# Performance work log

Hardware: AMD Instinct MI355X
Metric: run time of the kernel (lower is better)

The kernel has to match this reference:

```python
import jax, jax.numpy as jnp
import numpy as np
from jax import lax

NL, H, E, N, R, K, C, V, P = 8, 768, 1536, 16, 4, 4, 3, 256, 2048
EPS = 1e-5

def layernorm(x, w, b):
    m = jnp.mean(x, -1, keepdims=True)
    v = jnp.var(x, -1, keepdims=True)
    return (x - m) * lax.rsqrt(v + EPS) * w + b

def causal_dwconv(x, w, b):
    # x: [B,L,E], w: [E,K], b: [E]; causal depthwise conv (pad K-1 left, truncate)
    Bn, L, _ = x.shape
    xp = jnp.pad(x, ((0, 0), (K - 1, 0), (0, 0)))
    y = b
    acc = jnp.zeros_like(x)
    for j in range(K):
        acc = acc + xp[:, j:j + L, :] * w[:, j]
    return acc + b

def selective_scan(u, dt, Bm, Cm, A, Dv):
    # u,dt: [B,L,E]; Bm,Cm: [B,L,N]; A: [E,N]; Dv: [E]
    Bn = u.shape[0]
    def step(h, inp):
        u_t, dt_t, b_t, c_t = inp  # [B,E],[B,E],[B,N],[B,N]
        dA = jnp.exp(dt_t[:, :, None] * A)                      # [B,E,N]
        h = h * dA + (dt_t * u_t)[:, :, None] * b_t[:, None, :]
        y = jnp.einsum('ben,bn->be', h, c_t)
        return h, y
    h0 = jnp.zeros((Bn, E, N), dtype=u.dtype)
    xs = (u.transpose(1, 0, 2), dt.transpose(1, 0, 2),
          Bm.transpose(1, 0, 2), Cm.transpose(1, 0, 2))
    _, ys = lax.scan(step, h0, xs)
    return ys.transpose(1, 0, 2) + u * Dv

def mamba_block(hs, p):
    res = hs
    x = layernorm(hs, p['ln_w'], p['ln_b'])
    proj = x @ p['in_w'] + p['in_b']                            # [B,L,2E]
    xm, gate = proj[..., :E], proj[..., E:]
    xm = causal_dwconv(xm, p['conv_w'], p['conv_b'])
    u = jax.nn.silu(xm)                                         # swish activation in mixer
    dbc = u @ p['xproj_w']                                      # [B,L,R+2N]
    dt = jax.nn.softplus(dbc[..., :R] @ p['dt_w'] + p['dt_b'])  # [B,L,E]
    Bm, Cm = dbc[..., R:R + N], dbc[..., R + N:]
    A = -jnp.exp(p['A_log'])                                    # [E,N]
    y = selective_scan(u, dt, Bm, Cm, A, p['D'])
    y = jax.nn.sigmoid(gate) * y
    hs = y @ p['out_w'] + p['out_b'] + res
    # fractal layer: mean of recursive swish-linear branches, residual
    acc = jnp.zeros_like(hs)
    for i in range(C):
        yb = hs
        for _ in range(3):
            yb = jax.nn.silu(yb @ p['frac_w'][i] + p['frac_b'][i])
        acc = acc + yb
    return hs + 0.5 * acc / C

def setup_inputs() -> dict:
    key = jax.random.key(0)
    ks = jax.random.split(key, 20)
    s = lambda i, shp, sc=0.02: jax.random.normal(ks[i], shp, jnp.float32) * sc
    inp = {
        'input_ids': jax.random.randint(ks[0], (2, 2048), 0, V),
        'tok_emb': s(1, (V, H)),
        'pos_emb': s(2, (P, H)),
        'ln_w': jnp.ones((NL, H)), 'ln_b': jnp.zeros((NL, H)),
        'in_w': s(3, (NL, H, 2 * E)), 'in_b': jnp.zeros((NL, 2 * E)),
        'conv_w': s(4, (NL, E, K), 0.3), 'conv_b': jnp.zeros((NL, E)),
        'xproj_w': s(5, (NL, E, R + 2 * N)),
        'dt_w': s(6, (NL, R, E), 0.1),
        'dt_b': jnp.full((NL, E), -4.0),
        'A_log': jnp.tile(jnp.log(jnp.arange(1, N + 1, dtype=jnp.float32)), (NL, E, 1)),
        'D': jnp.ones((NL, E)),
        'out_w': s(7, (NL, E, H)), 'out_b': jnp.zeros((NL, H)),
        'frac_w': s(8, (NL, C, H, H)), 'frac_b': jnp.zeros((NL, C, H)),
        'fln_w': jnp.ones((H,)), 'fln_b': jnp.zeros((H,)),
    }
    return inp

def reference(input_ids, tok_emb, pos_emb, ln_w, ln_b, in_w, in_b, conv_w, conv_b,
              xproj_w, dt_w, dt_b, A_log, D, out_w, out_b, frac_w, frac_b, fln_w, fln_b):
    Bn, L = input_ids.shape
    hs = tok_emb[input_ids] + pos_emb[jnp.arange(L)][None]
    for l in range(NL):
        p = {'ln_w': ln_w[l], 'ln_b': ln_b[l], 'in_w': in_w[l], 'in_b': in_b[l],
             'conv_w': conv_w[l], 'conv_b': conv_b[l], 'xproj_w': xproj_w[l],
             'dt_w': dt_w[l], 'dt_b': dt_b[l], 'A_log': A_log[l], 'D': D[l],
             'out_w': out_w[l], 'out_b': out_b[l], 'frac_w': frac_w[l], 'frac_b': frac_b[l]}
        hs = mamba_block(hs, p)
    return layernorm(hs, fln_w, fln_b)
```

## Files before the change

kernel.cpp:

```cpp
#include <hip/hip_runtime.h>
#include <hip/hip_bf16.h>
#include <stdint.h>

#define NLAYER 8
#define HDIM   768
#define EDIM   1536
#define NST    16
#define LSEQ   2048
#define BATCH  2
#define BLTOK  (BATCH*LSEQ)
#define NCH    (BATCH*EDIM)
#define NCHK   64

typedef unsigned short u16;
typedef short  short8  __attribute__((ext_vector_type(8)));
typedef float  f32x4   __attribute__((ext_vector_type(4)));
typedef unsigned short u16x4 __attribute__((ext_vector_type(4)));

__device__ __forceinline__ float sigm(float x){ return 1.0f/(1.0f+__expf(-x)); }

__device__ __forceinline__ u16 bf16_rne(float x){
  unsigned u = __float_as_uint(x);
  return (u16)((u + 0x7fffu + ((u>>16)&1u)) >> 16);
}
__device__ __forceinline__ float bf16_f(u16 h){
  return __uint_as_float(((unsigned)h)<<16);
}

__device__ __forceinline__ void gload16(const void* g, void* l){
  __builtin_amdgcn_global_load_lds(
    reinterpret_cast<const __attribute__((address_space(1))) unsigned*>(
        reinterpret_cast<uintptr_t>(g)),
    reinterpret_cast<__attribute__((address_space(3))) unsigned*>(
        reinterpret_cast<uintptr_t>(l)),
    16, 0, 0);
}

__global__ __launch_bounds__(256) void wprep_k(
    const float* __restrict__ W, u16* __restrict__ H, u16* __restrict__ L,
    int Nsrc, int Ndst, int K)
{
  __shared__ float T[32][33];
  int z = blockIdx.z;
  W += (size_t)z*K*Nsrc; H += (size_t)z*Ndst*K; L += (size_t)z*Ndst*K;
  int n0 = blockIdx.x*32, k0 = blockIdx.y*32;
  int tx = threadIdx.x&31, ty = threadIdx.x>>5;
  #pragma unroll
  for (int r=0;r<4;r++){
    int kk = ty+8*r, col = n0+tx;
    T[kk][tx] = (col<Nsrc) ? W[(size_t)(k0+kk)*Nsrc+col] : 0.f;
  }
  __syncthreads();
  #pragma unroll
  for (int r=0;r<4;r++){
    int nn = ty+8*r, n = n0+nn, k = k0+tx;
    if (n<Ndst){
      float f = T[tx][nn];
      u16 h = bf16_rne(f);
      H[(size_t)n*K+k] = h;
      L[(size_t)n*K+k] = bf16_rne(f - bf16_f(h));
    }
  }
}

template<int EPI, int SPLIT, int SPLITK>
__global__ __launch_bounds__(256) void gemm_u(
    const u16* __restrict__ AH, const u16* __restrict__ AL, int lda,
    const u16* __restrict__ WH, const u16* __restrict__ WL, int ldw,
    const float* __restrict__ bias, void* __restrict__ Cout,
    int N, int Kloop, size_t zA, size_t zW, size_t zB, size_t zC)
{
  constexpr int NPL = (SPLIT==3)?4:2;
  __shared__ __align__(16) u16 smem[NPL*4096];
  u16* AsH = smem;
  u16* BsH = smem + 4096;
  u16* AsL = smem + 2*4096;
  u16* BsL = smem + 3*4096;

  const int z = blockIdx.z;
  const u16* ah = AH + (size_t)z*zA;
  const u16* bh = WH + (size_t)z*zW;
  const u16* al = nullptr;
  const u16* bl = nullptr;
  if constexpr (SPLIT==3){ al = AL + (size_t)z*zA; bl = WL + (size_t)z*zW; }

  const int tid  = threadIdx.x;
  const int m0 = blockIdx.y<<7, n0 = blockIdx.x<<7;
  const int wave = tid>>6, lane = tid&63;
  const int r = lane&15, q = lane>>4;
  const int wm = (wave&1)<<6, wn = (wave>>1)<<6;
  const int srow = tid>>2;
  const int scol = (tid&3)*8;
  const int sdst = tid*8;

  f32x4 acc[4][4];
  #pragma unroll
  for (int i=0;i<4;i++)
    #pragma unroll
    for (int j=0;j<4;j++)
      #pragma unroll
      for (int t=0;t<4;t++) acc[i][j][t]=0.f;

  for (int k0 = 0; k0 < Kloop; k0 += 32){
    #pragma unroll
    for (int i=0;i<2;i++){
      const size_t gao = (size_t)(m0 + i*64 + srow)*lda + k0 + scol;
      const size_t gbo = (size_t)(n0 + i*64 + srow)*ldw + k0 + scol;
      const int lo = i*2048 + sdst;
      gload16(ah+gao, AsH+lo);
      gload16(bh+gbo, BsH+lo);
      if constexpr (SPLIT==3){
        gload16(al+gao, AsL+lo);
        gload16(bl+gbo, BsL+lo);
      }
    }
    __syncthreads();

    short8 aHf[4], bHf[4];
    #pragma unroll
    for (int i=0;i<4;i++) aHf[i] = *(const short8*)&AsH[(wm + 16*i + r)*32 + q*8];
    #pragma unroll
    for (int j=0;j<4;j++) bHf[j] = *(const short8*)&BsH[(wn + 16*j + r)*32 + q*8];
    if constexpr (SPLIT==3){
      short8 aLf[4], bLf[4];
      #pragma unroll
      for (int i=0;i<4;i++) aLf[i] = *(const short8*)&AsL[(wm + 16*i + r)*32 + q*8];
      #pragma unroll
      for (int j=0;j<4;j++) bLf[j] = *(const short8*)&BsL[(wn + 16*j + r)*32 + q*8];
      #pragma unroll
      for (int i=0;i<4;i++)
        #pragma unroll
        for (int j=0;j<4;j++){
          acc[i][j] = __builtin_amdgcn_mfma_f32_16x16x32_bf16(aHf[i], bHf[j], acc[i][j], 0,0,0);
          acc[i][j] = __builtin_amdgcn_mfma_f32_16x16x32_bf16(aHf[i], bLf[j], acc[i][j], 0,0,0);
          acc[i][j] = __builtin_amdgcn_mfma_f32_16x16x32_bf16(aLf[i], bHf[j], acc[i][j], 0,0,0);
        }
    } else {
      #pragma unroll
      for (int i=0;i<4;i++)
        #pragma unroll
        for (int j=0;j<4;j++)
          acc[i][j] = __builtin_amdgcn_mfma_f32_16x16x32_bf16(aHf[i], bHf[j], acc[i][j], 0,0,0);
    }
    __syncthreads();
  }

  float* Cf = (float*)Cout + (size_t)z*zC;
  u16*   Cu = (u16*)Cout   + (size_t)z*zC;
  const float* bz = bias ? (bias + (size_t)z*zB) : bias;
  #pragma unroll
  for (int j=0;j<4;j++){
    int n_out = n0 + wn + 16*j + r;
    float bv = (bz && (!SPLITK || z==0)) ? bz[n_out] : 0.f;
    #pragma unroll
    for (int i=0;i<4;i++){
      #pragma unroll
      for (int reg=0;reg<4;reg++){
        int m_out = m0 + wm + 16*i + 4*q + reg;
        float v = acc[i][j][reg] + bv;
        if (EPI & 1) v *= sigm(v);
        size_t o = (size_t)m_out*N + n_out;
        if      (EPI & 16) atomicAdd(&Cf[o], v);
        else if (EPI & 8)  Cu[o] = bf16_rne(v);
        else if (EPI & 2)  Cf[o] += v;
        else               Cf[o] = v;
      }
    }
  }
}

__global__ __launch_bounds__(64) void xgemm_k(
    const float* __restrict__ A, const u16* __restrict__ XH,
    const u16* __restrict__ XL, float* __restrict__ DBC)
{
  int m0 = blockIdx.x*16;
  int lane = threadIdx.x;
  int r = lane&15, q = lane>>4;
  f32x4 acc[3];
  #pragma unroll
  for (int j=0;j<3;j++)
    #pragma unroll
    for (int t=0;t<4;t++) acc[j][t]=0.f;

  for (int k0 = 0; k0 < EDIM; k0 += 32){
    const float* ap = A + (size_t)(m0+r)*EDIM + k0 + q*8;
    float f[8];
    *(float4*)&f[0] = *(const float4*)(ap+0);
    *(float4*)&f[4] = *(const float4*)(ap+4);
    short8 ah, al;
    #pragma unroll
    for (int t=0;t<8;t++){
      u16 h = bf16_rne(f[t]);
      ah[t] = (short)h;
      al[t] = (short)bf16_rne(f[t]-bf16_f(h));
    }
    #pragma unroll
    for (int j=0;j<3;j++){
      size_t o = (size_t)(16*j+r)*EDIM + k0 + q*8;
      short8 bh = *(const short8*)&XH[o];
      short8 bl = *(const short8*)&XL[o];
      acc[j] = __builtin_amdgcn_mfma_f32_16x16x32_bf16(ah, bh, acc[j], 0,0,0);
      acc[j] = __builtin_amdgcn_mfma_f32_16x16x32_bf16(ah, bl, acc[j], 0,0,0);
      acc[j] = __builtin_amdgcn_mfma_f32_16x16x32_bf16(al, bh, acc[j], 0,0,0);
    }
  }
  #pragma unroll
  for (int j=0;j<3;j++){
    int n = 16*j + r;
    if (n < 36){
      #pragma unroll
      for (int reg=0;reg<4;reg++){
        int m = m0 + 4*q + reg;
        DBC[(size_t)m*36 + n] = acc[j][reg];
      }
    }
  }
}

__global__ __launch_bounds__(256) void embed_k(
    const int* __restrict__ ids, const float* __restrict__ tok,
    const float* __restrict__ pos, float* __restrict__ HS)
{
  int idx = blockIdx.x*256 + threadIdx.x;
  int h = idx % HDIM; int t = idx / HDIM;
  int lpos = t % LSEQ;
  int id = ids[t];
  HS[idx] = tok[id*HDIM + h] + pos[lpos*HDIM + h];
}

template<int PACK>
__global__ __launch_bounds__(256) void ln_k(
    const float* __restrict__ X, const float* __restrict__ w,
    const float* __restrict__ b, void* __restrict__ O1, void* __restrict__ O2)
{
  int t = blockIdx.x;
  const float* x = X + (size_t)t*HDIM;
  float s=0.f, s2=0.f;
  for (int i=threadIdx.x; i<HDIM; i+=256){ float v=x[i]; s+=v; s2+=v*v; }
  #pragma unroll
  for (int off=32; off; off>>=1){ s += __shfl_down(s,off,64); s2 += __shfl_down(s2,off,64); }
  __shared__ float rs[4], rs2[4], mv[2];
  int lane = threadIdx.x & 63, wv = threadIdx.x >> 6;
  if (!lane){ rs[wv]=s; rs2[wv]=s2; }
  __syncthreads();
  if (!threadIdx.x){
    float a = rs[0]+rs[1]+rs[2]+rs[3];
    float c = rs2[0]+rs2[1]+rs2[2]+rs2[3];
    float m = a/HDIM;
    mv[0]=m; mv[1]=rsqrtf(c/HDIM - m*m + 1e-5f);
  }
  __syncthreads();
  float m = mv[0], r = mv[1];
  for (int i=threadIdx.x; i<HDIM; i+=256){
    float v = (x[i]-m)*r*w[i] + b[i];
    if (PACK){
      u16 h = bf16_rne(v);
      ((u16*)O1)[(size_t)t*HDIM+i] = h;
      ((u16*)O2)[(size_t)t*HDIM+i] = bf16_rne(v - bf16_f(h));
    } else {
      ((float*)O1)[(size_t)t*HDIM+i] = v;
    }
  }
}

__global__ __launch_bounds__(256) void cvt_k(
    const float* __restrict__ X, u16* __restrict__ O)
{
  int i = blockIdx.x*256 + threadIdx.x;
  float4 v = ((const float4*)X)[i];
  u16x4 o;
  o[0]=bf16_rne(v.x); o[1]=bf16_rne(v.y); o[2]=bf16_rne(v.z); o[3]=bf16_rne(v.w);
  ((u16x4*)O)[i] = o;
}

__global__ __launch_bounds__(256) void conv_silu_k(
    const float* __restrict__ PROJ, const float* __restrict__ cw,
    const float* __restrict__ cb, float* __restrict__ U)
{
  int idx = blockIdx.x*256 + threadIdx.x;
  int e = idx % EDIM; int t = idx / EDIM;
  int l = t % LSEQ; int tb = t - l;
  float acc = cb[e];
  #pragma unroll
  for (int j=0;j<4;j++){
    int tt = l + j - 3;
    if (tt >= 0) acc += PROJ[(size_t)(tb+tt)*(2*EDIM) + e] * cw[e*4+j];
  }
  U[idx] = acc * sigm(acc);
}

__global__ __launch_bounds__(256) void scanA_k(
    const float* __restrict__ U, const float* __restrict__ DBC,
    const float* __restrict__ Alog, const float* __restrict__ dtw,
    const float* __restrict__ dtb, float* __restrict__ PSP,
    float* __restrict__ PSS)
{
  const int CH = LSEQ/NCHK;
  int el = threadIdx.x & 63, jj = threadIdx.x >> 6;
  int ch = blockIdx.x*64 + el;
  int j  = blockIdx.y*4 + jj;
  int e = ch % EDIM, b = ch / EDIM;

  float a[16], P[16], S[16];
  #pragma unroll
  for (int n=0;n<16;n++){ a[n] = -__expf(Alog[e*NST+n]); P[n]=1.f; S[n]=0.f; }
  float w0=dtw[e], w1=dtw[EDIM+e], w2=dtw[2*EDIM+e], w3=dtw[3*EDIM+e];
  float db=dtb[e];
  size_t base=(size_t)b*LSEQ;

  for (int t=j*CH; t<j*CH+CH; t++){
    size_t tok = base+t;
    float4 d4 = *(const float4*)&DBC[tok*36];
    float4 B0 = *(const float4*)&DBC[tok*36+4];
    float4 B1 = *(const float4*)&DBC[tok*36+8];
    float4 B2 = *(const float4*)&DBC[tok*36+12];
    float4 B3 = *(const float4*)&DBC[tok*36+16];
    float dt = d4.x*w0 + d4.y*w1 + d4.z*w2 + d4.w*w3 + db;
    dt = (dt>20.f)?dt:log1pf(__expf(dt));
    float du = dt * U[tok*EDIM+e];
    float Bv[16];
    *(float4*)&Bv[0]=B0; *(float4*)&Bv[4]=B1; *(float4*)&Bv[8]=B2; *(float4*)&Bv[12]=B3;
    #pragma unroll
    for (int n=0;n<16;n++){
      float dA = __expf(dt*a[n]);
      P[n]*=dA; S[n]=S[n]*dA + du*Bv[n];
    }
  }
  #pragma unroll
  for (int n=0;n<16;n++){
    PSP[(size_t)(j*16+n)*NCH + ch] = P[n];
    PSS[(size_t)(j*16+n)*NCH + ch] = S[n];
  }
}

__global__ __launch_bounds__(256) void scanB_k(
    const float* __restrict__ PSP, float* __restrict__ PSS)
{
  int idx = blockIdx.x*256 + threadIdx.x;
  int n = idx / NCH, ch = idx % NCH;
  float hin = 0.f;
  #pragma unroll 4
  for (int jj=0;jj<NCHK;jj++){
    size_t o = (size_t)(jj*16+n)*NCH + ch;
    float p = PSP[o], s = PSS[o];
    PSS[o] = hin;
    hin = p*hin + s;
  }
}

__global__ __launch_bounds__(256) void scanC_k(
    const float* __restrict__ U, const float* __restrict__ DBC,
    const float* __restrict__ Alog, const float* __restrict__ dtw,
    const float* __restrict__ dtb, const float* __restrict__ HIN,
    const float* __restrict__ Dp, const float* __restrict__ PROJ,
    u16* __restrict__ YH, u16* __restrict__ YL)
{
  const int CH = LSEQ/NCHK;
  int el = threadIdx.x & 63, jj = threadIdx.x >> 6;
  int ch = blockIdx.x*64 + el;
  int j  = blockIdx.y*4 + jj;
  int e = ch % EDIM, b = ch / EDIM;

  float a[16], h[16];
  #pragma unroll
  for (int n=0;n<16;n++){
    a[n] = -__expf(Alog[e*NST+n]);
    h[n] = HIN[(size_t)(j*16+n)*NCH + ch];
  }
  float w0=dtw[e], w1=dtw[EDIM+e], w2=dtw[2*EDIM+e], w3=dtw[3*EDIM+e];
  float db=dtb[e], dcf=Dp[e];
  size_t base=(size_t)b*LSEQ;

  for (int t=j*CH; t<j*CH+CH; t++){
    size_t tok = base+t;
    float4 d4 = *(const float4*)&DBC[tok*36];
    float4 B0 = *(const float4*)&DBC[tok*36+4];
    float4 B1 = *(const float4*)&DBC[tok*36+8];
    float4 B2 = *(const float4*)&DBC[tok*36+12];
    float4 B3 = *(const float4*)&DBC[tok*36+16];
    float4 C0 = *(const float4*)&DBC[tok*36+20];
    float4 C1 = *(const float4*)&DBC[tok*36+24];
    float4 C2 = *(const float4*)&DBC[tok*36+28];
    float4 C3 = *(const float4*)&DBC[tok*36+32];
    float dt = d4.x*w0 + d4.y*w1 + d4.z*w2 + d4.w*w3 + db;
    dt = (dt>20.f)?dt:log1pf(__expf(dt));
    float u = U[tok*EDIM+e];
    float du = dt * u;
    float Bv[16], Cv[16];
    *(float4*)&Bv[0]=B0; *(float4*)&Bv[4]=B1; *(float4*)&Bv[8]=B2; *(float4*)&Bv[12]=B3;
    *(float4*)&Cv[0]=C0; *(float4*)&Cv[4]=C1; *(float4*)&Cv[8]=C2; *(float4*)&Cv[12]=C3;
    float y = 0.f;
    #pragma unroll
    for (int n=0;n<16;n++){
      float dA = __expf(dt*a[n]);
      h[n] = h[n]*dA + du*Bv[n];
      y += h[n]*Cv[n];
    }
    float g = PROJ[tok*(2*EDIM) + EDIM + e];
    float yv = (y + u*dcf)*sigm(g);
    u16 hh = bf16_rne(yv);
    YH[tok*EDIM + e] = hh;
    YL[tok*EDIM + e] = bf16_rne(yv - bf16_f(hh));
  }
}

__global__ __launch_bounds__(256) void addscale3_k(
    float* __restrict__ HS, const float* __restrict__ FB)
{
  const size_t S = (size_t)BLTOK*HDIM;
  size_t i = blockIdx.x*256 + threadIdx.x;
  HS[i] += (FB[i] + FB[i+S] + FB[i+2*S]) * (0.5f/3.0f);
}

extern "C" void kernel_launch(void* const* d_in, const int* in_sizes, int n_in,
                              void* d_out, int out_size, void* d_ws, size_t ws_size,
                              hipStream_t stream)
{
  const int*   ids      = (const int*)d_in[0];
  const float* tok_emb  = (const float*)d_in[1];
  const float* pos_emb  = (const float*)d_in[2];
  const float* ln_w     = (const float*)d_in[3];
  const float* ln_b     = (const float*)d_in[4];
  const float* in_w     = (const float*)d_in[5];
  const float* in_b     = (const float*)d_in[6];
  const float* conv_w   = (const float*)d_in[7];
  const float* conv_b   = (const float*)d_in[8];
  const float* xproj_w  = (const float*)d_in[9];
  const float* dt_w     = (const float*)d_in[10];
  const float* dt_b     = (const float*)d_in[11];
  const float* A_log    = (const float*)d_in[12];
  const float* Dp       = (const float*)d_in[13];
  const float* out_w    = (const float*)d_in[14];
  const float* out_b    = (const float*)d_in[15];
  const float* frac_w   = (const float*)d_in[16];
  const float* frac_b   = (const float*)d_in[17];
  const float* fln_w    = (const float*)d_in[18];
  const float* fln_b    = (const float*)d_in[19];

  const size_t F_HS   = (size_t)BLTOK*HDIM;
  const size_t F_PROJ = (size_t)BLTOK*2*EDIM;
  const size_t F_R1   = (size_t)BLTOK*EDIM;
  float* HS   = (float*)d_ws;
  float* PROJ = HS   + F_HS;
  float* R1   = PROJ + F_PROJ;
  float* DBC  = R1   + F_R1;
  u16* W16  = (u16*)(DBC + (size_t)BLTOK*36);
  u16* inH  = W16;
  u16* inL  = inH  + (size_t)2359296;
  u16* outH = inL  + (size_t)2359296;
  u16* outL = outH + (size_t)1179648;
  u16* frH  = outL + (size_t)1179648;
  u16* frL  = frH  + (size_t)1769472;
  u16* xH   = frL  + (size_t)1769472;
  u16* xL   = xH   + (size_t)73728;
  float* PSP = (float*)(xL + (size_t)73728);
  float* PSS = PSP + (size_t)NCHK*16*NCH;
  u16* YH  = (u16*)(PSS + (size_t)NCHK*16*NCH);
  u16* YL  = YH + (size_t)BLTOK*EDIM;
  u16*   XH  = (u16*)R1;
  u16*   XL  = XH + F_HS;
  float* U   = R1;
  u16*   HSB = (u16*)PSP;
  float* FB  = PROJ;
  u16*   S1  = (u16*)(PROJ + 3*F_HS);
  u16*   S2  = S1 + 3*F_HS;

  embed_k<<<(BLTOK*HDIM)/256, 256, 0, stream>>>(ids, tok_emb, pos_emb, HS);

  const size_t zWf = (size_t)HDIM*HDIM;
  for (int l = 0; l < NLAYER; l++){
    wprep_k<<<dim3(3072/32, 768/32), 256, 0, stream>>>(
        in_w + (size_t)l*HDIM*2*EDIM, inH, inL, 2*EDIM, 2*EDIM, HDIM);
    wprep_k<<<dim3(768/32, 1536/32), 256, 0, stream>>>(
        out_w + (size_t)l*EDIM*HDIM, outH, outL, HDIM, HDIM, EDIM);
    wprep_k<<<dim3(768/32, 768/32, 3), 256, 0, stream>>>(
        frac_w + (size_t)l*3*HDIM*HDIM, frH, frL, HDIM, HDIM, HDIM);
    wprep_k<<<dim3(2, 1536/32), 256, 0, stream>>>(
        xproj_w + (size_t)l*EDIM*36, xH, xL, 36, 48, EDIM);

    ln_k<1><<<BLTOK, 256, 0, stream>>>(HS, ln_w + l*HDIM, ln_b + l*HDIM, XH, XL);

    gemm_u<0,3,0><<<dim3(24, 32), 256, 0, stream>>>(
        XH, XL, HDIM, inH, inL, HDIM, in_b + l*2*EDIM, PROJ,
        2*EDIM, HDIM, 0,0,0,0);

    conv_silu_k<<<(BLTOK*EDIM)/256, 256, 0, stream>>>(
        PROJ, conv_w + l*EDIM*4, conv_b + l*EDIM, U);

    xgemm_k<<<BLTOK/16, 64, 0, stream>>>(U, xH, xL, DBC);

    scanA_k<<<dim3(NCH/64, NCHK/4), 256, 0, stream>>>(
        U, DBC, A_log + (size_t)l*EDIM*NST, dt_w + (size_t)l*4*EDIM,
        dt_b + (size_t)l*EDIM, PSP, PSS);
    scanB_k<<<(NCH*16)/256, 256, 0, stream>>>(PSP, PSS);
    scanC_k<<<dim3(NCH/64, NCHK/4), 256, 0, stream>>>(
        U, DBC, A_log + (size_t)l*EDIM*NST, dt_w + (size_t)l*4*EDIM,
        dt_b + (size_t)l*EDIM, PSS, Dp + (size_t)l*EDIM, PROJ, YH, YL);

    gemm_u<16,3,1><<<dim3(6, 32, 2), 256, 0, stream>>>(
        YH, YL, EDIM, outH, outL, EDIM, out_b + l*HDIM, HS,
        HDIM, EDIM/2, EDIM/2, EDIM/2, 0, 0);

    cvt_k<<<(BLTOK*HDIM)/1024, 256, 0, stream>>>(HS, HSB);

    gemm_u<9,1,0><<<dim3(6, 32, 3), 256, 0, stream>>>(
        HSB, nullptr, HDIM, frH, frL, HDIM, frac_b + (size_t)l*3*HDIM, S1,
        HDIM, HDIM, 0, zWf, HDIM, F_HS);
    gemm_u<9,1,0><<<dim3(6, 32, 3), 256, 0, stream>>>(
        S1, nullptr, HDIM, frH, frL, HDIM, frac_b + (size_t)l*3*HDIM, S2,
        HDIM, HDIM, F_HS, zWf, HDIM, F_HS);
    gemm_u<1,1,0><<<dim3(6, 32, 3), 256, 0, stream>>>(
        S2, nullptr, HDIM, frH, frL, HDIM, frac_b + (size_t)l*3*HDIM, FB,
        HDIM, HDIM, F_HS, zWf, HDIM, F_HS);

    addscale3_k<<<(BLTOK*HDIM)/256, 256, 0, stream>>>(HS, FB);
  }

  ln_k<0><<<BLTOK, 256, 0, stream>>>(HS, fln_w, fln_b, (float*)d_out, nullptr);
}
```

Before: 4.057 ms.

## Double-buffer GEMM shared-memory tiles to overlap global loads with MFMA

The GEMM now keeps two shared-memory stages and issues direct-to-LDS global loads for tile k+2 while computing tile k. It waits on vmcnt so only the current stage must be complete, reads the fragments into registers, and then barriers so the freed buffer can be refilled. The goal is to hide global memory latency behind the matrix-core work that was previously serialized by load→sync→compute. The cost is doubled LDS use, which may lower occupancy, and a dependence on hand-counted vmcnt values.

```diff
diff --git a/kernel.cpp b/kernel.cpp
--- a/kernel.cpp
+++ b/kernel.cpp
@@ -71,11 +71,8 @@
     int N, int Kloop, size_t zA, size_t zW, size_t zB, size_t zC)
 {
   constexpr int NPL = (SPLIT==3)?4:2;
-  __shared__ __align__(16) u16 smem[NPL*4096];
-  u16* AsH = smem;
-  u16* BsH = smem + 4096;
-  u16* AsL = smem + 2*4096;
-  u16* BsL = smem + 3*4096;
+  constexpr int NLD = (SPLIT==3)?8:4;
+  __shared__ __align__(16) u16 smem[2*NPL*4096];
 
   const int z = blockIdx.z;
   const u16* ah = AH + (size_t)z*zA;
@@ -93,40 +90,66 @@
   const int scol = (tid&3)*8;
   const int sdst = tid*8;
 
-  f32x4 acc[4][4];
-  #pragma unroll
-  for (int i=0;i<4;i++)
-    #pragma unroll
-    for (int j=0;j<4;j++)
-      #pragma unroll
-      for (int t=0;t<4;t++) acc[i][j][t]=0.f;
-
-  for (int k0 = 0; k0 < Kloop; k0 += 32){
+  const int nk = Kloop >> 5;
+
+  auto STAGE = [&](int idx){
+    u16* s = smem + (size_t)(idx&1)*NPL*4096;
+    const int k0 = idx<<5;
     #pragma unroll
     for (int i=0;i<2;i++){
       const size_t gao = (size_t)(m0 + i*64 + srow)*lda + k0 + scol;
       const size_t gbo = (size_t)(n0 + i*64 + srow)*ldw + k0 + scol;
       const int lo = i*2048 + sdst;
-      gload16(ah+gao, AsH+lo);
-      gload16(bh+gbo, BsH+lo);
+      gload16(ah+gao, s+lo);
+      gload16(bh+gbo, s+4096+lo);
       if constexpr (SPLIT==3){
-        gload16(al+gao, AsL+lo);
-        gload16(bl+gbo, BsL+lo);
+        gload16(al+gao, s+2*4096+lo);
+        gload16(bl+gbo, s+3*4096+lo);
       }
     }
-    __syncthreads();
+  };
+
+  f32x4 acc[4][4];
+  #pragma unroll
+  for (int i=0;i<4;i++)
+    #pragma unroll
+    for (int j=0;j<4;j++)
+      #pragma unroll
+      for (int t=0;t<4;t++) acc[i][j][t]=0.f;
+
+  STAGE(0);
+  if (nk > 1) STAGE(1);
+
+  for (int idx = 0; idx < nk; idx++){
+    if (idx+1 < nk) asm volatile("s_waitcnt vmcnt(%0)" :: "n"(NLD) : "memory");
+    else            asm volatile("s_waitcnt vmcnt(0)" ::: "memory");
+    __builtin_amdgcn_s_barrier();
+
+    const u16* s = smem + (size_t)(idx&1)*NPL*4096;
+    const u16* sA = s;
+    const u16* sB = s + 4096;
 
     short8 aHf[4], bHf[4];
     #pragma unroll
-    for (int i=0;i<4;i++) aHf[i] = *(const short8*)&AsH[(wm + 16*i + r)*32 + q*8];
-    #pragma unroll
-    for (int j=0;j<4;j++) bHf[j] = *(const short8*)&BsH[(wn + 16*j + r)*32 + q*8];
+    for (int i=0;i<4;i++) aHf[i] = *(const short8*)&sA[(wm + 16*i + r)*32 + q*8];
+    #pragma unroll
+    for (int j=0;j<4;j++) bHf[j] = *(const short8*)&sB[(wn + 16*j + r)*32 + q*8];
+    short8 aLf[4], bLf[4];
     if constexpr (SPLIT==3){
-      short8 aLf[4], bLf[4];
-      #pragma unroll
-      for (int i=0;i<4;i++) aLf[i] = *(const short8*)&AsL[(wm + 16*i + r)*32 + q*8];
-      #pragma unroll
-      for (int j=0;j<4;j++) bLf[j] = *(const short8*)&BsL[(wn + 16*j + r)*32 + q*8];
+      const u16* sAL = s + 2*4096;
+      const u16* sBL = s + 3*4096;
+      #pragma unroll
+      for (int i=0;i<4;i++) aLf[i] = *(const short8*)&sAL[(wm + 16*i + r)*32 + q*8];
+      #pragma unroll
+      for (int j=0;j<4;j++) bLf[j] = *(const short8*)&sBL[(wn + 16*j + r)*32 + q*8];
+    }
+    asm volatile("s_waitcnt lgkmcnt(0)" ::: "memory");
+    __builtin_amdgcn_sched_barrier(0);
+    __builtin_amdgcn_s_barrier();
+
+    if (idx+2 < nk) STAGE(idx+2);
+
+    if constexpr (SPLIT==3){
       #pragma unroll
       for (int i=0;i<4;i++)
         #pragma unroll
@@ -142,7 +165,6 @@
         for (int j=0;j<4;j++)
           acc[i][j] = __builtin_amdgcn_mfma_f32_16x16x32_bf16(aHf[i], bHf[j], acc[i][j], 0,0,0);
     }
-    __syncthreads();
   }
 
   float* Cf = (float*)Cout + (size_t)z*zC;
```

Result: faster. 3.855 ms (-5.0%).
